# Kernel tuning notes

Hardware: AMD Instinct MI355X
Metric: run time of the kernel (lower is better)

The kernel has to match this reference:

```python
import jax, jax.numpy as jnp
import numpy as np

EMB, VOCAB, HID, STY = 512, 32000, 1024, 512
B, L = 32, 64

def setup_inputs() -> dict:
    key = jax.random.key(0)
    ks = jax.random.split(key, 16)
    s = 0.02  # small init to keep gates unsaturated
    return {
        'rnn_inputs': jax.random.randint(ks[0], (B, L), 0, VOCAB),
        'sentence_vector': jax.random.normal(ks[1], (B, HID), dtype=jnp.float32) * 0.1,
        'embed': jax.random.normal(ks[2], (VOCAB, EMB), dtype=jnp.float32) * s,
        'U_w': jax.random.normal(ks[3], (EMB, 4 * STY), dtype=jnp.float32) * s,
        'U_b': jnp.zeros((4 * STY,), dtype=jnp.float32),
        'S1_w': jax.random.normal(ks[4], (4 * STY, STY), dtype=jnp.float32) * s,
        'S1_b': jnp.zeros((STY,), dtype=jnp.float32),
        'V_w': jax.random.normal(ks[5], (STY, 4 * HID), dtype=jnp.float32) * s,
        'V_b': jnp.zeros((4 * HID,), dtype=jnp.float32),
        'W_w': jax.random.normal(ks[6], (HID, 4 * HID), dtype=jnp.float32) * s,
        'W_b': jnp.zeros((4 * HID,), dtype=jnp.float32),
        'P_w': jax.random.normal(ks[7], (HID, VOCAB), dtype=jnp.float32) * s,
        'P_b': jnp.zeros((VOCAB,), dtype=jnp.float32),
    }

def reference(rnn_inputs, sentence_vector, embed, U_w, U_b, S1_w, S1_b,
              V_w, V_b, W_w, W_b, P_w, P_b):
    emb = embed[rnn_inputs]                     # [B, L, E]
    xs = jnp.swapaxes(emb[:, :-1, :], 0, 1)     # time-major [L-1, B, E]
    h0 = sentence_vector
    c0 = sentence_vector

    def step(carry, x):
        h, c = carry
        U = x @ U_w + U_b                       # [B, 4*STY]
        S = U @ S1_w + S1_b                     # [B, STY]  (mode='default')
        g = (S @ V_w + V_b) + (h @ W_w + W_b)   # [B, 4*HID]
        i, f, o, cg = jnp.split(g, 4, axis=1)   # split order i, f, o, c
        c_new = jax.nn.sigmoid(f) * c + jax.nn.sigmoid(i) * jnp.tanh(cg)
        h_new = jax.nn.sigmoid(o) * c_new
        out = h_new @ P_w + P_b                 # [B, VOCAB]
        return (h_new, c_new), out

    _, outs = jax.lax.scan(step, (h0, c0), xs)  # [L-1, B, VOCAB]
    return jnp.swapaxes(outs, 0, 1)             # [B, L-1, VOCAB]
```

## Files before the change

### kernel.cpp

```cpp
#include <hip/hip_runtime.h>
#include <hip/hip_bf16.h>


typedef __bf16 bf16;
typedef bf16 bf16x8 __attribute__((ext_vector_type(8)));
typedef float f32x4 __attribute__((ext_vector_type(4)));

#define NB 32
#define NL 64
#define NT 63
#define NE 512
#define NS4 2048
#define NS 512
#define NH 1024
#define NG 4096
#define NV 32000
#define MPAD 2048

#define RNB 32
#define FSTR 32

__device__ __forceinline__ float sigmoidf_(float x) { return 1.0f / (1.0f + expf(-x)); }

__device__ __forceinline__ void gload_lds16(const bf16* g, bf16* l) {
  __builtin_amdgcn_global_load_lds(
      (const __attribute__((address_space(1))) unsigned int*)g,
      (__attribute__((address_space(3))) unsigned int*)l, 16, 0, 0);
}

__global__ void k_transpose_cvt(const float* __restrict__ src, bf16* __restrict__ dst,
                                int R, int C) {
  __shared__ float t[32][33];
  int bx = blockIdx.x * 32;
  int by = blockIdx.y * 32;
  int tx = threadIdx.x & 31, ty = threadIdx.x >> 5;
#pragma unroll
  for (int i = 0; i < 32; i += 8)
    t[ty + i][tx] = src[(size_t)(by + ty + i) * C + (bx + tx)];
  __syncthreads();
#pragma unroll
  for (int i = 0; i < 32; i += 8)
    dst[(size_t)(bx + ty + i) * R + (by + tx)] = (bf16)t[tx][ty + i];
}

__global__ void k_gather(const int* __restrict__ rnn, const float* __restrict__ embed,
                         bf16* __restrict__ X) {
  int r = blockIdx.x;
  if (r < NB * NT) {
    int t = r >> 5, b = r & 31;
    int tok = rnn[b * NL + t];
    const float* src = embed + (size_t)tok * NE;
    for (int e = threadIdx.x; e < NE; e += 256) X[(size_t)r * NE + e] = (bf16)src[e];
  } else {
    for (int e = threadIdx.x; e < NE; e += 256) X[(size_t)r * NE + e] = (bf16)0.0f;
  }
}

__global__ void k_init(const float* __restrict__ sv, bf16* __restrict__ h0,
                       unsigned* __restrict__ flags) {
  int i = blockIdx.x * 256 + threadIdx.x;
  if (i < RNB * FSTR) flags[i] = 0u;
  if (i < NB * NH) h0[i] = (bf16)sv[i];
}

__global__ void k_bias2(const float* __restrict__ a, const float* __restrict__ b,
                        float* __restrict__ o) {
  int i = blockIdx.x * 256 + threadIdx.x;
  if (i < NG) o[i] = a[i] + b[i];
}

template <int OUT_MODE>
__global__ __launch_bounds__(256, 2) void k_gemm(const bf16* __restrict__ A,
                                                 const bf16* __restrict__ Bt,
                                                 const float* __restrict__ bias,
                                                 void* __restrict__ Cp, int K, int N) {
  __shared__ bf16 As[128 * 32];
  __shared__ bf16 Bs[128 * 32];
  const int tid = threadIdx.x;
  const int m0 = blockIdx.y * 128, n0 = blockIdx.x * 128;
  const int lane = tid & 63, w = tid >> 6;
  const int l15 = lane & 15, kq = lane >> 4;
  const int m_off = (w & 1) * 64, n_off = (w >> 1) * 64;
  const int c0 = 2 * w, c1 = 2 * w + 1;
  const int sub = lane >> 2, kkl = (lane & 3) * 8;
  const bf16* pA0 = A + (size_t)(m0 + c0 * 16 + sub) * K + kkl;
  const bf16* pA1 = A + (size_t)(m0 + c1 * 16 + sub) * K + kkl;
  const bf16* pB0 = Bt + (size_t)(n0 + c0 * 16 + sub) * K + kkl;
  const bf16* pB1 = Bt + (size_t)(n0 + c1 * 16 + sub) * K + kkl;
  f32x4 acc[4][4] = {};
  for (int k0 = 0; k0 < K; k0 += 32) {
    __syncthreads();
    gload_lds16(pA0 + k0, &As[c0 * 512]);
    gload_lds16(pA1 + k0, &As[c1 * 512]);
    gload_lds16(pB0 + k0, &Bs[c0 * 512]);
    gload_lds16(pB1 + k0, &Bs[c1 * 512]);
    __syncthreads();
    bf16x8 a[4], b[4];
#pragma unroll
    for (int i = 0; i < 4; i++)
      a[i] = *(const bf16x8*)&As[(m_off + 16 * i + l15) * 32 + kq * 8];
#pragma unroll
    for (int j = 0; j < 4; j++)
      b[j] = *(const bf16x8*)&Bs[(n_off + 16 * j + l15) * 32 + kq * 8];
#pragma unroll
    for (int i = 0; i < 4; i++)
#pragma unroll
      for (int j = 0; j < 4; j++)
        acc[i][j] = __builtin_amdgcn_mfma_f32_16x16x32_bf16(a[i], b[j], acc[i][j], 0, 0, 0);
  }
#pragma unroll
  for (int j = 0; j < 4; j++) {
    const int col = n0 + n_off + 16 * j + l15;
    const float bv = bias[col];
#pragma unroll
    for (int i = 0; i < 4; i++) {
#pragma unroll
      for (int r = 0; r < 4; r++) {
        const int row = m0 + m_off + 16 * i + kq * 4 + r;
        const float v = acc[i][j][r] + bv;
        if (OUT_MODE == 0) {
          ((bf16*)Cp)[(size_t)row * N + col] = (bf16)v;
        } else if (OUT_MODE == 1) {
          ((float*)Cp)[(size_t)row * N + col] = v;
        } else {
          if (row < NB * NT) {
            int t = row >> 5, b = row & 31;
            ((float*)Cp)[((size_t)b * NT + t) * NV + col] = v;
          }
        }
      }
    }
  }
}

__global__ __launch_bounds__(512) void k_rnn(const bf16* __restrict__ Wt,
                                             const float* __restrict__ Gx,
                                             const float* __restrict__ sv,
                                             bf16* __restrict__ hb,
                                             unsigned* __restrict__ flags) {
  __shared__ bf16 hs[32 * 1032];
  __shared__ float gl[4][32][32];
  __shared__ float cs[32][32];
  const int tid = threadIdx.x;
  const int lane = tid & 63, wid = tid >> 6;
  const int g = wid & 3, ch = wid >> 2;
  const int l15 = lane & 15, kq = lane >> 4;
  const int j0 = blockIdx.x * 32;
  const int bb_e = tid >> 4, jj_e = tid & 15;

  cs[bb_e][jj_e] = sv[bb_e * NH + j0 + jj_e];
  cs[bb_e][jj_e + 16] = sv[bb_e * NH + j0 + jj_e + 16];

  const bf16* wrow = Wt + (size_t)(g * NH + j0 + ch * 16 + l15) * NH;
  bf16x8 breg[32];
#pragma unroll
  for (int k = 0; k < 32; k++) breg[k] = *(const bf16x8*)&wrow[k * 32 + kq * 8];

  for (int t = 0; t < NT; t++) {
    const float* gx0 = Gx + (size_t)t * NB * NG + (size_t)bb_e * NG + j0;
    float gxr[8];
#pragma unroll
    for (int u = 0; u < 2; u++)
#pragma unroll
      for (int gg = 0; gg < 4; gg++)
        gxr[u * 4 + gg] = gx0[gg * NH + jj_e + u * 16];
    const bf16* hp = hb + (size_t)t * NB * NH;
#pragma unroll
    for (int q = 0; q < 8; q++) {
      int idx = tid + 512 * q;
      int row = idx >> 7, col = (idx & 127) * 8;
      *(bf16x8*)&hs[row * 1032 + col] = *(const bf16x8*)&hp[row * NH + col];
    }
    __syncthreads();
    f32x4 acc0 = {}, acc1 = {};
#pragma unroll
    for (int k = 0; k < 32; k++) {
      bf16x8 a0 = *(const bf16x8*)&hs[l15 * 1032 + k * 32 + kq * 8];
      bf16x8 a1 = *(const bf16x8*)&hs[(16 + l15) * 1032 + k * 32 + kq * 8];
      acc0 = __builtin_amdgcn_mfma_f32_16x16x32_bf16(a0, breg[k], acc0, 0, 0, 0);
      acc1 = __builtin_amdgcn_mfma_f32_16x16x32_bf16(a1, breg[k], acc1, 0, 0, 0);
    }
#pragma unroll
    for (int r = 0; r < 4; r++) {
      gl[g][kq * 4 + r][ch * 16 + l15] = acc0[r];
      gl[g][16 + kq * 4 + r][ch * 16 + l15] = acc1[r];
    }
    __syncthreads();
    bf16* hw = hb + (size_t)(t + 1) * NB * NH + (size_t)bb_e * NH + j0;
#pragma unroll
    for (int u = 0; u < 2; u++) {
      const int jj = jj_e + u * 16;
      float gi = gl[0][bb_e][jj] + gxr[u * 4 + 0];
      float gf = gl[1][bb_e][jj] + gxr[u * 4 + 1];
      float go = gl[2][bb_e][jj] + gxr[u * 4 + 2];
      float gc = gl[3][bb_e][jj] + gxr[u * 4 + 3];
      float cp = cs[bb_e][jj];
      float cn = sigmoidf_(gf) * cp + sigmoidf_(gi) * tanhf(gc);
      float hn = sigmoidf_(go) * cn;
      cs[bb_e][jj] = cn;
      hw[jj] = (bf16)hn;
    }
    if (t + 1 < NT) {
      __syncthreads();
      if (wid == 0) {
        __builtin_amdgcn_fence(__ATOMIC_RELEASE, "agent");
        if (lane == 0)
          __hip_atomic_store(&flags[blockIdx.x * FSTR], (unsigned)(t + 1),
                             __ATOMIC_RELAXED, __HIP_MEMORY_SCOPE_AGENT);
        const unsigned tgt = (unsigned)(t + 1);
        for (;;) {
          unsigned v = __hip_atomic_load(&flags[(lane & 31) * FSTR],
                                         __ATOMIC_RELAXED, __HIP_MEMORY_SCOPE_AGENT);
          if (__all((int)(v >= tgt))) break;
          __builtin_amdgcn_s_sleep(1);
        }
        __builtin_amdgcn_fence(__ATOMIC_ACQUIRE, "agent");
      }
      __syncthreads();
    }
  }
}

extern "C" void kernel_launch(void* const* d_in, const int* in_sizes, int n_in,
                              void* d_out, int out_size, void* d_ws, size_t ws_size,
                              hipStream_t stream) {
  const int* rnn = (const int*)d_in[0];
  const float* sv = (const float*)d_in[1];
  const float* embed = (const float*)d_in[2];
  const float* U_w = (const float*)d_in[3];
  const float* U_b = (const float*)d_in[4];
  const float* S1_w = (const float*)d_in[5];
  const float* S1_b = (const float*)d_in[6];
  const float* V_w = (const float*)d_in[7];
  const float* V_b = (const float*)d_in[8];
  const float* W_w = (const float*)d_in[9];
  const float* W_b = (const float*)d_in[10];
  const float* P_w = (const float*)d_in[11];
  const float* P_b = (const float*)d_in[12];
  float* out = (float*)d_out;

  char* ws = (char*)d_ws;
  size_t off = 0;
  auto alloc = [&](size_t bytes) -> void* {
    void* p = ws + off;
    off += (bytes + 255) & ~(size_t)255;
    return p;
  };
  bf16* Pt = (bf16*)alloc((size_t)NV * NH * 2);
  float* Gx = (float*)alloc((size_t)MPAD * NG * 4);
  bf16* Ub = (bf16*)alloc((size_t)MPAD * NS4 * 2);
  bf16* Wt = (bf16*)alloc((size_t)NG * NH * 2);
  bf16* hb = (bf16*)alloc((size_t)(MPAD + 32) * NH * 2);
  bf16* Vt = (bf16*)alloc((size_t)NG * NS * 2);
  bf16* Xb = (bf16*)alloc((size_t)MPAD * NE * 2);
  bf16* Ut = (bf16*)alloc((size_t)NS4 * NE * 2);
  bf16* S1t = (bf16*)alloc((size_t)NS * NS4 * 2);
  bf16* Sb = (bf16*)alloc((size_t)MPAD * NS * 2);
  float* vbwb = (float*)alloc((size_t)NG * 4);
  unsigned* flags = (unsigned*)alloc((size_t)RNB * FSTR * 4);
  (void)in_sizes; (void)n_in; (void)out_size; (void)ws_size;

  k_transpose_cvt<<<dim3(NS4 / 32, NE / 32), 256, 0, stream>>>(U_w, Ut, NE, NS4);
  k_transpose_cvt<<<dim3(NS / 32, NS4 / 32), 256, 0, stream>>>(S1_w, S1t, NS4, NS);
  k_transpose_cvt<<<dim3(NG / 32, NS / 32), 256, 0, stream>>>(V_w, Vt, NS, NG);
  k_transpose_cvt<<<dim3(NG / 32, NH / 32), 256, 0, stream>>>(W_w, Wt, NH, NG);
  k_transpose_cvt<<<dim3(NV / 32, NH / 32), 256, 0, stream>>>(P_w, Pt, NH, NV);
  k_bias2<<<NG / 256, 256, 0, stream>>>(V_b, W_b, vbwb);
  k_init<<<(NB * NH + 255) / 256, 256, 0, stream>>>(sv, hb, flags);
  k_gather<<<MPAD, 256, 0, stream>>>(rnn, embed, Xb);

  k_gemm<0><<<dim3(NS4 / 128, MPAD / 128), 256, 0, stream>>>(Xb, Ut, U_b, Ub, NE, NS4);
  k_gemm<0><<<dim3(NS / 128, MPAD / 128), 256, 0, stream>>>(Ub, S1t, S1_b, Sb, NS4, NS);
  k_gemm<1><<<dim3(NG / 128, MPAD / 128), 256, 0, stream>>>(Sb, Vt, vbwb, Gx, NS, NG);

  k_rnn<<<RNB, 512, 0, stream>>>(Wt, Gx, sv, hb, flags);

  k_gemm<2><<<dim3(NV / 128, MPAD / 128), 256, 0, stream>>>(hb + (size_t)NB * NH, Pt,
                                                            P_b, out, NH, NV);
}
```

Before: 1.040 ms.

## Replace agent fences with write-through h stores and lighter barriers in RNN loop

The recurrent kernel now has each thread compute two adjacent hidden units and write them as one packed dword. The store uses an inline-asm global_store_dword with sc0 sc1 cache bits so the data goes out write-through. This lets the code drop the release/acquire agent fences and the s_sleep in the inter-block flag spin, using s_waitcnt vmcnt(0) plus raw s_barrier instead. LDS gate and cell arrays are padded to stride 33 to avoid bank conflicts, and the Gx loads become float2 vector loads. This relies on the cache-bit semantics being enough for cross-CU visibility without an acquire fence, which is a memory-ordering correctness risk.

```diff
diff --git a/kernel.cpp b/kernel.cpp
--- a/kernel.cpp
+++ b/kernel.cpp
@@ -5,6 +5,7 @@
 typedef __bf16 bf16;
 typedef bf16 bf16x8 __attribute__((ext_vector_type(8)));
 typedef float f32x4 __attribute__((ext_vector_type(4)));
+typedef float f32x2 __attribute__((ext_vector_type(2)));
 
 #define NB 32
 #define NL 64
@@ -26,6 +27,10 @@
   __builtin_amdgcn_global_load_lds(
       (const __attribute__((address_space(1))) unsigned int*)g,
       (__attribute__((address_space(3))) unsigned int*)l, 16, 0, 0);
+}
+
+__device__ __forceinline__ void store_dword_wt(void* p, unsigned v) {
+  asm volatile("global_store_dword %0, %1, off sc0 sc1" ::"v"(p), "v"(v) : "memory");
 }
 
 __global__ void k_transpose_cvt(const float* __restrict__ src, bf16* __restrict__ dst,
@@ -139,17 +144,19 @@
                                              bf16* __restrict__ hb,
                                              unsigned* __restrict__ flags) {
   __shared__ bf16 hs[32 * 1032];
-  __shared__ float gl[4][32][32];
-  __shared__ float cs[32][32];
+  __shared__ float gl[4][32][33];
+  __shared__ float cs[32][33];
   const int tid = threadIdx.x;
   const int lane = tid & 63, wid = tid >> 6;
   const int g = wid & 3, ch = wid >> 2;
   const int l15 = lane & 15, kq = lane >> 4;
   const int j0 = blockIdx.x * 32;
-  const int bb_e = tid >> 4, jj_e = tid & 15;
-
-  cs[bb_e][jj_e] = sv[bb_e * NH + j0 + jj_e];
-  cs[bb_e][jj_e + 16] = sv[bb_e * NH + j0 + jj_e + 16];
+  const int bb_e = tid >> 4;
+  const int jp = tid & 15;
+  const int c0e = 2 * jp, c1e = 2 * jp + 1;
+
+  cs[bb_e][c0e] = sv[bb_e * NH + j0 + c0e];
+  cs[bb_e][c1e] = sv[bb_e * NH + j0 + c1e];
 
   const bf16* wrow = Wt + (size_t)(g * NH + j0 + ch * 16 + l15) * NH;
   bf16x8 breg[32];
@@ -157,13 +164,10 @@
   for (int k = 0; k < 32; k++) breg[k] = *(const bf16x8*)&wrow[k * 32 + kq * 8];
 
   for (int t = 0; t < NT; t++) {
-    const float* gx0 = Gx + (size_t)t * NB * NG + (size_t)bb_e * NG + j0;
-    float gxr[8];
-#pragma unroll
-    for (int u = 0; u < 2; u++)
-#pragma unroll
-      for (int gg = 0; gg < 4; gg++)
-        gxr[u * 4 + gg] = gx0[gg * NH + jj_e + u * 16];
+    const float* gx0 = Gx + (size_t)t * NB * NG + (size_t)bb_e * NG + j0 + c0e;
+    f32x2 gxr[4];
+#pragma unroll
+    for (int gg = 0; gg < 4; gg++) gxr[gg] = *(const f32x2*)&gx0[gg * NH];
     const bf16* hp = hb + (size_t)t * NB * NH;
 #pragma unroll
     for (int q = 0; q < 8; q++) {
@@ -186,24 +190,30 @@
       gl[g][16 + kq * 4 + r][ch * 16 + l15] = acc1[r];
     }
     __syncthreads();
-    bf16* hw = hb + (size_t)(t + 1) * NB * NH + (size_t)bb_e * NH + j0;
-#pragma unroll
-    for (int u = 0; u < 2; u++) {
-      const int jj = jj_e + u * 16;
-      float gi = gl[0][bb_e][jj] + gxr[u * 4 + 0];
-      float gf = gl[1][bb_e][jj] + gxr[u * 4 + 1];
-      float go = gl[2][bb_e][jj] + gxr[u * 4 + 2];
-      float gc = gl[3][bb_e][jj] + gxr[u * 4 + 3];
-      float cp = cs[bb_e][jj];
-      float cn = sigmoidf_(gf) * cp + sigmoidf_(gi) * tanhf(gc);
-      float hn = sigmoidf_(go) * cn;
-      cs[bb_e][jj] = cn;
-      hw[jj] = (bf16)hn;
+    {
+      float hn2[2];
+#pragma unroll
+      for (int u = 0; u < 2; u++) {
+        const int jj = c0e + u;
+        float gi = gl[0][bb_e][jj] + gxr[0][u];
+        float gf = gl[1][bb_e][jj] + gxr[1][u];
+        float go = gl[2][bb_e][jj] + gxr[2][u];
+        float gc = gl[3][bb_e][jj] + gxr[3][u];
+        float cp = cs[bb_e][jj];
+        float cn = sigmoidf_(gf) * cp + sigmoidf_(gi) * tanhf(gc);
+        hn2[u] = sigmoidf_(go) * cn;
+        cs[bb_e][jj] = cn;
+      }
+      unsigned short b0 = __builtin_bit_cast(unsigned short, (bf16)hn2[0]);
+      unsigned short b1 = __builtin_bit_cast(unsigned short, (bf16)hn2[1]);
+      unsigned pv = (unsigned)b0 | ((unsigned)b1 << 16);
+      bf16* hw = hb + (size_t)(t + 1) * NB * NH + (size_t)bb_e * NH + j0 + c0e;
+      store_dword_wt(hw, pv);
     }
     if (t + 1 < NT) {
-      __syncthreads();
+      asm volatile("s_waitcnt vmcnt(0)" ::: "memory");
+      __builtin_amdgcn_s_barrier();
       if (wid == 0) {
-        __builtin_amdgcn_fence(__ATOMIC_RELEASE, "agent");
         if (lane == 0)
           __hip_atomic_store(&flags[blockIdx.x * FSTR], (unsigned)(t + 1),
                              __ATOMIC_RELAXED, __HIP_MEMORY_SCOPE_AGENT);
@@ -212,11 +222,10 @@
           unsigned v = __hip_atomic_load(&flags[(lane & 31) * FSTR],
                                          __ATOMIC_RELAXED, __HIP_MEMORY_SCOPE_AGENT);
           if (__all((int)(v >= tgt))) break;
-          __builtin_amdgcn_s_sleep(1);
         }
-        __builtin_amdgcn_fence(__ATOMIC_ACQUIRE, "agent");
       }
-      __syncthreads();
+      __builtin_amdgcn_s_barrier();
+      asm volatile("" ::: "memory");
     }
   }
 }
```

New measurement: 1.007 ms. 3.2% less time.
